# Kernel optimization log

Measured on AMD Instinct MI355X. Metric: run time of the kernel, lower is better.

## Reference

```python
import jax, jax.numpy as jnp
import numpy as np

N_NODES = 50000
N_EDGES = 800000
NFEAT, NHID, NCLASS = 256, 64, 40


def setup_inputs() -> dict:
    key = jax.random.key(0)
    ks = jax.random.split(key, 8)
    x = jax.random.normal(ks[0], (N_NODES, NFEAT), dtype=jnp.float32)
    W1 = jax.random.normal(ks[1], (NFEAT, NHID), dtype=jnp.float32) * (1.0 / np.sqrt(NFEAT))
    b1 = jax.random.normal(ks[2], (NHID,), dtype=jnp.float32) * 0.01
    W2 = jax.random.normal(ks[3], (NHID, NCLASS), dtype=jnp.float32) * (1.0 / np.sqrt(NHID))
    b2 = jax.random.normal(ks[4], (NCLASS,), dtype=jnp.float32) * 0.01
    edge_weight = jax.random.uniform(ks[5], (N_EDGES,), dtype=jnp.float32)
    edge_src = jax.random.randint(ks[6], (N_EDGES,), 0, N_NODES)
    edge_dst = jax.random.randint(ks[7], (N_EDGES,), 0, N_NODES)
    return {"x": x, "W1": W1, "b1": b1, "W2": W2, "b2": b2,
            "edge_weight": edge_weight, "edge_src": edge_src, "edge_dst": edge_dst}


def reference(x, W1, b1, W2, b2, edge_weight, edge_src, edge_dst):
    n = x.shape[0]

    def spmm(h):  # sparse adj @ h via gather + weighted segment-sum
        msgs = h[edge_src] * edge_weight[:, None]  # [E, d]
        return jax.ops.segment_sum(msgs, edge_dst, num_segments=n)

    # gc1: adj @ (x @ W1) + b1, then relu (dropout is identity in eval mode)
    h = jax.nn.relu(spmm(x @ W1) + b1)
    # gc2: adj @ (h @ W2) + b2
    logits = spmm(h @ W2) + b2
    return (logits, jax.nn.log_softmax(logits, axis=1))
```

## Files before the change

kernel.cpp:

```cpp
#include <hip/hip_runtime.h>
#include <math.h>

#define N_NODES 50000
#define N_EDGES 800000
#define NFEAT 256
#define NHID 64
#define NCLASS 40
#define NPB 16
#define NB  3125
#define CAP 512
#define NC 98
#define CAPC 16384
#define BIN_EPB 8192
#define NBIN 98
#define NGEMM 782
#define ACC2S 68

typedef __attribute__((ext_vector_type(8))) short bf16x8;
typedef __attribute__((ext_vector_type(4))) float f32x4;

__device__ __forceinline__ ushort f2bf(float f) {
    unsigned u = __float_as_uint(f);
    u += 0x7FFF + ((u >> 16) & 1);
    return (ushort)(u >> 16);
}
__device__ __forceinline__ float bf2f(ushort us) {
    return __uint_as_float(((unsigned)us) << 16);
}

__global__ __launch_bounds__(256) void k_prep(const float* __restrict__ W1,
                                              const float* __restrict__ W2,
                                              ushort* __restrict__ W1f,
                                              ushort* __restrict__ W2f) {
    int idx = blockIdx.x * 256 + threadIdx.x;
    if (idx < 2048) {
        int lane = idx & 63, ctks = idx >> 6;
        int ks = ctks & 7, ct = ctks >> 3;
        int col = ct * 16 + (lane & 15);
        int r0 = ks * 32 + (lane >> 4) * 8;
        bf16x8 frag;
        #pragma unroll
        for (int j = 0; j < 8; ++j) frag[j] = (short)f2bf(W1[(r0 + j) * NHID + col]);
        *(bf16x8*)&W1f[(size_t)idx * 8] = frag;
    } else if (idx < 2048 + 384) {
        int i2 = idx - 2048;
        int lane = i2 & 63, ctks = i2 >> 6;
        int ks = ctks & 1, ct = ctks >> 1;
        int col = ct * 16 + (lane & 15);
        int r0 = ks * 32 + (lane >> 4) * 8;
        bf16x8 frag;
        #pragma unroll
        for (int j = 0; j < 8; ++j)
            frag[j] = (short)((col < NCLASS) ? f2bf(W2[(r0 + j) * NCLASS + col]) : 0);
        *(bf16x8*)&W2f[(size_t)i2 * 8] = frag;
    }
}

__global__ __launch_bounds__(1024) void k_mega(const int* __restrict__ esrc,
                                               const int* __restrict__ edst,
                                               const float* __restrict__ ewt,
                                               int* __restrict__ bfillc,
                                               int2* __restrict__ coarse,
                                               const float* __restrict__ x,
                                               const ushort* __restrict__ W1f,
                                               ushort* __restrict__ xW1b) {
    __shared__ __align__(16) char smem[64 * 256 * 2];
    int tid = threadIdx.x;

    if (blockIdx.x < NBIN) {
        int* cnt  = (int*)smem;
        int* base = cnt + NC;
        for (int i = tid; i < NC; i += 1024) cnt[i] = 0;
        __syncthreads();
        int eb = blockIdx.x * BIN_EPB;
        #pragma unroll
        for (int k = 0; k < BIN_EPB; k += 1024) {
            int e = eb + k + tid;
            if (e < N_EDGES) atomicAdd(&cnt[edst[e] >> 9], 1);
        }
        __syncthreads();
        for (int i = tid; i < NC; i += 1024) {
            int c = cnt[i];
            base[i] = c ? atomicAdd(&bfillc[i], c) : 0;
            cnt[i] = 0;
        }
        __syncthreads();
        #pragma unroll
        for (int k = 0; k < BIN_EPB; k += 1024) {
            int e = eb + k + tid;
            if (e < N_EDGES) {
                int d = edst[e];
                int c = d >> 9;
                int pos = base[c] + atomicAdd(&cnt[c], 1);
                coarse[(size_t)c * CAPC + pos] =
                    make_int2(esrc[e] | ((d & 511) << 16), __float_as_int(ewt[e]));
            }
        }
        return;
    }

    ushort* sX = (ushort*)smem;
    int w = tid >> 6, lane = tid & 63;
    int ct = w & 3, rg = w >> 2;
    int row0 = (blockIdx.x - NBIN) * 64;

    bf16x8 Bf[8];
    #pragma unroll
    for (int ks = 0; ks < 8; ++ks)
        Bf[ks] = *(const bf16x8*)&W1f[(size_t)((ct * 8 + ks) * 64 + lane) * 8];

    {
        int row = tid & 63;
        int colbase = (tid >> 6) * 16;
        int crow = min(row0 + row, N_NODES - 1);
        const float* xp = x + (size_t)crow * NFEAT + colbase;
        #pragma unroll
        for (int c2 = 0; c2 < 2; ++c2) {
            float4 v0 = *(const float4*)(xp + c2 * 8);
            float4 v1 = *(const float4*)(xp + c2 * 8 + 4);
            bf16x8 fr;
            fr[0] = (short)f2bf(v0.x); fr[1] = (short)f2bf(v0.y);
            fr[2] = (short)f2bf(v0.z); fr[3] = (short)f2bf(v0.w);
            fr[4] = (short)f2bf(v1.x); fr[5] = (short)f2bf(v1.y);
            fr[6] = (short)f2bf(v1.z); fr[7] = (short)f2bf(v1.w);
            int chunk = colbase / 8 + c2;
            *(bf16x8*)&sX[row * 256 + ((chunk ^ (row & 7)) * 8)] = fr;
        }
    }
    __syncthreads();

    f32x4 acc = {0.f, 0.f, 0.f, 0.f};
    int arow = rg * 16 + (lane & 15);
    #pragma unroll
    for (int ks = 0; ks < 8; ++ks) {
        int chunk = ks * 4 + (lane >> 4);
        bf16x8 Af = *(const bf16x8*)&sX[arow * 256 + ((chunk ^ (arow & 7)) * 8)];
        acc = __builtin_amdgcn_mfma_f32_16x16x32_bf16(Af, Bf[ks], acc, 0, 0, 0);
    }
    int col = ct * 16 + (lane & 15);
    int rbase = row0 + rg * 16 + (lane >> 4) * 4;
    #pragma unroll
    for (int r = 0; r < 4; ++r) {
        int row = rbase + r;
        if (row < N_NODES)
            xW1b[(size_t)row * NHID + col] = f2bf(acc[r]);
    }
}

__global__ __launch_bounds__(512) void k_passB(const int* __restrict__ bfillc,
                                               const int2* __restrict__ coarse,
                                               int* __restrict__ bfill,
                                               int2* __restrict__ binned) {
    __shared__ int cnt[32];
    __shared__ int base[32];
    int tid = threadIdx.x;
    int c = blockIdx.x >> 1;
    int half = blockIdx.x & 1;
    int fillc = bfillc[c];
    int h0 = (fillc + 1) >> 1;
    int js = c * CAPC + half * h0;
    int je = c * CAPC + (half ? fillc : h0);

    if (tid < 32) cnt[tid] = 0;
    __syncthreads();
    for (int j = js + tid; j < je; j += 512) {
        int dstlow = (coarse[j].x >> 16) & 511;
        atomicAdd(&cnt[dstlow >> 4], 1);
    }
    __syncthreads();
    if (tid < 32) {
        int cc = cnt[tid];
        base[tid] = cc ? atomicAdd(&bfill[c * 32 + tid], cc) : 0;
        cnt[tid] = 0;
    }
    __syncthreads();
    for (int j = js + tid; j < je; j += 512) {
        int2 p = coarse[j];
        int dstlow = (p.x >> 16) & 511;
        int fb = dstlow >> 4;
        int pos = base[fb] + atomicAdd(&cnt[fb], 1);
        binned[(size_t)(c * 32 + fb) * CAP + pos] =
            make_int2((p.x & 0xFFFF) | ((dstlow & 15) << 16), p.y);
    }
}

__global__ __launch_bounds__(256) void k_spmm1b(const ushort* __restrict__ xW1b,
                                                const int* __restrict__ bfill,
                                                const int2* __restrict__ binned,
                                                const float* __restrict__ b1,
                                                ushort* __restrict__ h_b) {
    __shared__ float accs[4][NPB * NHID];
    int wv = threadIdx.x >> 6, lane = threadIdx.x & 63;
    int b = blockIdx.x;
    float* acc = accs[wv];
    #pragma unroll
    for (int n = 0; n < NPB; ++n) acc[n * NHID + lane] = 0.f;

    int s = b * CAP, e = s + bfill[b];
    int len = e - s;
    int q = (len + 3) >> 2;
    int j = s + wv * q;
    int je = min(j + q, e);
    for (; j + 8 <= je; j += 8) {
        int2 p[8];
        #pragma unroll
        for (int k = 0; k < 8; ++k) p[k] = binned[j + k];
        float g[8];
        #pragma unroll
        for (int k = 0; k < 8; ++k)
            g[k] = bf2f(xW1b[(p[k].x & 0xFFFF) * NHID + lane]);
        #pragma unroll
        for (int k = 0; k < 8; ++k)
            acc[(p[k].x >> 16) * NHID + lane] += __int_as_float(p[k].y) * g[k];
    }
    for (; j < je; ++j) {
        int2 p0 = binned[j];
        float g0 = bf2f(xW1b[(p0.x & 0xFFFF) * NHID + lane]);
        acc[(p0.x >> 16) * NHID + lane] += __int_as_float(p0.y) * g0;
    }
    __syncthreads();

    float bias = b1[lane];
    #pragma unroll
    for (int i = 0; i < 4; ++i) {
        int n = wv * 4 + i;
        float v = accs[0][n * NHID + lane] + accs[1][n * NHID + lane]
                + accs[2][n * NHID + lane] + accs[3][n * NHID + lane] + bias;
        h_b[(size_t)(b * NPB + n) * NHID + lane] = f2bf(v > 0.f ? v : 0.f);
    }
}

__global__ __launch_bounds__(256) void k_spmm2f(const ushort* __restrict__ h_b,
                                                const int* __restrict__ bfill,
                                                const int2* __restrict__ binned,
                                                const ushort* __restrict__ W2f,
                                                const float* __restrict__ b2,
                                                float* __restrict__ out) {
    __shared__ float accs[4][NPB * ACC2S];
    int wv = threadIdx.x >> 6, lane = threadIdx.x & 63;
    int b = blockIdx.x;
    float* acc = accs[wv];
    #pragma unroll
    for (int n = 0; n < NPB; ++n) acc[n * ACC2S + lane] = 0.f;

    int s = b * CAP, e = s + bfill[b];
    int len = e - s;
    int q = (len + 3) >> 2;
    int j = s + wv * q;
    int je = min(j + q, e);
    for (; j + 8 <= je; j += 8) {
        int2 p[8];
        #pragma unroll
        for (int k = 0; k < 8; ++k) p[k] = binned[j + k];
        float g[8];
        #pragma unroll
        for (int k = 0; k < 8; ++k)
            g[k] = bf2f(h_b[(p[k].x & 0xFFFF) * NHID + lane]);
        #pragma unroll
        for (int k = 0; k < 8; ++k)
            acc[(p[k].x >> 16) * ACC2S + lane] += __int_as_float(p[k].y) * g[k];
    }
    for (; j < je; ++j) {
        int2 p0 = binned[j];
        float g0 = bf2f(h_b[(p0.x & 0xFFFF) * NHID + lane]);
        acc[(p0.x >> 16) * ACC2S + lane] += __int_as_float(p0.y) * g0;
    }
    __syncthreads();

    for (int i = threadIdx.x; i < NPB * 64; i += 256) {
        int idx = (i >> 6) * ACC2S + (i & 63);
        accs[0][idx] = accs[0][idx] + accs[1][idx] + accs[2][idx] + accs[3][idx];
    }
    __syncthreads();
    if (wv != 0) return;

    bf16x8 Af[2];
    #pragma unroll
    for (int ks = 0; ks < 2; ++ks) {
        const float* ap = &accs[0][(lane & 15) * ACC2S + ks * 32 + (lane >> 4) * 8];
        #pragma unroll
        for (int jj = 0; jj < 8; ++jj) Af[ks][jj] = (short)f2bf(ap[jj]);
    }
    f32x4 cv[3] = {{0.f,0.f,0.f,0.f},{0.f,0.f,0.f,0.f},{0.f,0.f,0.f,0.f}};
    #pragma unroll
    for (int ct = 0; ct < 3; ++ct) {
        #pragma unroll
        for (int ks = 0; ks < 2; ++ks) {
            bf16x8 Bf = *(const bf16x8*)&W2f[(size_t)((ct * 2 + ks) * 64 + lane) * 8];
            cv[ct] = __builtin_amdgcn_mfma_f32_16x16x32_bf16(Af[ks], Bf, cv[ct], 0, 0, 0);
        }
    }
    int colg = lane & 15;
    int g = lane >> 4;
    float bc0 = b2[colg];
    float bc1 = b2[16 + colg];
    float bc2 = (colg < 8) ? b2[32 + colg] : 0.f;
    #pragma unroll
    for (int i = 0; i < 4; ++i) {
        int node = b * NPB + g * 4 + i;
        float v0 = cv[0][i] + bc0;
        float v1 = cv[1][i] + bc1;
        float v2 = (colg < 8) ? (cv[2][i] + bc2) : -INFINITY;
        float m = fmaxf(fmaxf(v0, v1), v2);
        #pragma unroll
        for (int off = 1; off < 16; off <<= 1) m = fmaxf(m, __shfl_xor(m, off));
        float ex = __expf(v0 - m) + __expf(v1 - m) + ((colg < 8) ? __expf(v2 - m) : 0.f);
        #pragma unroll
        for (int off = 1; off < 16; off <<= 1) ex += __shfl_xor(ex, off);
        float ls = __logf(ex) + m;
        float* o0 = out + (size_t)node * NCLASS;
        float* o1 = o0 + (size_t)N_NODES * NCLASS;
        o0[colg] = v0;            o1[colg] = v0 - ls;
        o0[16 + colg] = v1;       o1[16 + colg] = v1 - ls;
        if (colg < 8) { o0[32 + colg] = v2;  o1[32 + colg] = v2 - ls; }
    }
}


extern "C" void kernel_launch(void* const* d_in, const int* in_sizes, int n_in,
                              void* d_out, int out_size, void* d_ws, size_t ws_size,
                              hipStream_t stream) {
    const float* x    = (const float*)d_in[0];
    const float* W1   = (const float*)d_in[1];
    const float* b1   = (const float*)d_in[2];
    const float* W2   = (const float*)d_in[3];
    const float* b2   = (const float*)d_in[4];
    const float* ewt  = (const float*)d_in[5];
    const int*   esrc = (const int*)d_in[6];
    const int*   edst = (const int*)d_in[7];
    float* out = (float*)d_out;

    char* p = (char*)d_ws;
    ushort* xW1b = (ushort*)p;   p += (size_t)N_NODES * NHID * 2;
    ushort* h_b  = (ushort*)p;   p += (size_t)N_NODES * NHID * 2;
    int2*   binned = (int2*)p;   p += (size_t)NB * CAP * 8 + 64;
    int2*   coarse = (int2*)p;   p += (size_t)NC * CAPC * 8;
    ushort* W1f  = (ushort*)p;   p += 2048 * 8 * 2;
    ushort* W2f  = (ushort*)p;   p += 384 * 8 * 2;
    int* bfillc  = (int*)p;      p += NC * 4;
    int* bfill   = (int*)p;      p += NB * 4;

    hipMemsetAsync(bfillc, 0, (NC + NB) * sizeof(int), stream);

    k_prep<<<10, 256, 0, stream>>>(W1, W2, W1f, W2f);
    k_mega<<<NBIN + NGEMM, 1024, 0, stream>>>(esrc, edst, ewt, bfillc, coarse,
                                              x, W1f, xW1b);
    k_passB<<<NC * 2, 512, 0, stream>>>(bfillc, coarse, bfill, binned);
    k_spmm1b<<<NB, 256, 0, stream>>>(xW1b, bfill, binned, b1, h_b);
    k_spmm2f<<<NB, 256, 0, stream>>>(h_b, bfill, binned, W2f, b2, out);
}
```

Measured before the change: 189.4 us.

## Apply W2 before second SpMM to shrink gathered feature width

The h@W2 projection moves out of the second SpMM epilogue and into the first SpMM's epilogue, using MFMA. It writes a 48-wide bf16 hW2 (40 classes padded) instead of the 64-wide h. The second SpMM then gathers 48-column rows, which cuts gather bytes per edge, and it performs bias plus log_softmax with a wave-wide reduction. The cost is an extra MFMA stage in spmm1, one more block barrier, and padded lanes that still load (clamped to column 0) in spmm2.

```diff
diff --git a/kernel.cpp b/kernel.cpp
--- a/kernel.cpp
+++ b/kernel.cpp
@@ -14,7 +14,8 @@
 #define BIN_EPB 8192
 #define NBIN 98
 #define NGEMM 782
-#define ACC2S 68
+#define NW2 48
+#define ACC1S 68
 
 typedef __attribute__((ext_vector_type(8))) short bf16x8;
 typedef __attribute__((ext_vector_type(4))) float f32x4;
@@ -188,13 +189,14 @@
                                                 const int* __restrict__ bfill,
                                                 const int2* __restrict__ binned,
                                                 const float* __restrict__ b1,
-                                                ushort* __restrict__ h_b) {
-    __shared__ float accs[4][NPB * NHID];
+                                                const ushort* __restrict__ W2f,
+                                                ushort* __restrict__ hW2b) {
+    __shared__ float accs[4][NPB * ACC1S];
     int wv = threadIdx.x >> 6, lane = threadIdx.x & 63;
     int b = blockIdx.x;
     float* acc = accs[wv];
     #pragma unroll
-    for (int n = 0; n < NPB; ++n) acc[n * NHID + lane] = 0.f;
+    for (int n = 0; n < NPB; ++n) acc[n * ACC1S + lane] = 0.f;
 
     int s = b * CAP, e = s + bfill[b];
     int len = e - s;
@@ -211,12 +213,12 @@
             g[k] = bf2f(xW1b[(p[k].x & 0xFFFF) * NHID + lane]);
         #pragma unroll
         for (int k = 0; k < 8; ++k)
-            acc[(p[k].x >> 16) * NHID + lane] += __int_as_float(p[k].y) * g[k];
+            acc[(p[k].x >> 16) * ACC1S + lane] += __int_as_float(p[k].y) * g[k];
     }
     for (; j < je; ++j) {
         int2 p0 = binned[j];
         float g0 = bf2f(xW1b[(p0.x & 0xFFFF) * NHID + lane]);
-        acc[(p0.x >> 16) * NHID + lane] += __int_as_float(p0.y) * g0;
+        acc[(p0.x >> 16) * ACC1S + lane] += __int_as_float(p0.y) * g0;
     }
     __syncthreads();
 
@@ -224,24 +226,53 @@
     #pragma unroll
     for (int i = 0; i < 4; ++i) {
         int n = wv * 4 + i;
-        float v = accs[0][n * NHID + lane] + accs[1][n * NHID + lane]
-                + accs[2][n * NHID + lane] + accs[3][n * NHID + lane] + bias;
-        h_b[(size_t)(b * NPB + n) * NHID + lane] = f2bf(v > 0.f ? v : 0.f);
-    }
-}
-
-__global__ __launch_bounds__(256) void k_spmm2f(const ushort* __restrict__ h_b,
+        int idx = n * ACC1S + lane;
+        float v = accs[0][idx] + accs[1][idx] + accs[2][idx] + accs[3][idx] + bias;
+        accs[0][idx] = v > 0.f ? v : 0.f;
+    }
+    __syncthreads();
+    if (wv != 0) return;
+
+    bf16x8 Af[2];
+    #pragma unroll
+    for (int ks = 0; ks < 2; ++ks) {
+        const float* ap = &accs[0][(lane & 15) * ACC1S + ks * 32 + (lane >> 4) * 8];
+        #pragma unroll
+        for (int jj = 0; jj < 8; ++jj) Af[ks][jj] = (short)f2bf(ap[jj]);
+    }
+    f32x4 cv[3] = {{0.f,0.f,0.f,0.f},{0.f,0.f,0.f,0.f},{0.f,0.f,0.f,0.f}};
+    #pragma unroll
+    for (int ct = 0; ct < 3; ++ct) {
+        #pragma unroll
+        for (int ks = 0; ks < 2; ++ks) {
+            bf16x8 Bf = *(const bf16x8*)&W2f[(size_t)((ct * 2 + ks) * 64 + lane) * 8];
+            cv[ct] = __builtin_amdgcn_mfma_f32_16x16x32_bf16(Af[ks], Bf, cv[ct], 0, 0, 0);
+        }
+    }
+    int colg = lane & 15;
+    int g = lane >> 4;
+    #pragma unroll
+    for (int i = 0; i < 4; ++i) {
+        int node = b * NPB + g * 4 + i;
+        ushort* o = hW2b + (size_t)node * NW2;
+        o[colg]      = f2bf(cv[0][i]);
+        o[16 + colg] = f2bf(cv[1][i]);
+        o[32 + colg] = f2bf(cv[2][i]);
+    }
+}
+
+__global__ __launch_bounds__(256) void k_spmm2g(const ushort* __restrict__ hW2b,
                                                 const int* __restrict__ bfill,
                                                 const int2* __restrict__ binned,
-                                                const ushort* __restrict__ W2f,
                                                 const float* __restrict__ b2,
                                                 float* __restrict__ out) {
-    __shared__ float accs[4][NPB * ACC2S];
+    __shared__ float accs[4][NPB * 64];
     int wv = threadIdx.x >> 6, lane = threadIdx.x & 63;
     int b = blockIdx.x;
     float* acc = accs[wv];
-    #pragma unroll
-    for (int n = 0; n < NPB; ++n) acc[n * ACC2S + lane] = 0.f;
+    int lf = lane < NW2 ? lane : 0;
+    #pragma unroll
+    for (int n = 0; n < NPB; ++n) acc[n * 64 + lane] = 0.f;
 
     int s = b * CAP, e = s + bfill[b];
     int len = e - s;
@@ -255,64 +286,38 @@
         float g[8];
         #pragma unroll
         for (int k = 0; k < 8; ++k)
-            g[k] = bf2f(h_b[(p[k].x & 0xFFFF) * NHID + lane]);
+            g[k] = bf2f(hW2b[(p[k].x & 0xFFFF) * NW2 + lf]);
         #pragma unroll
         for (int k = 0; k < 8; ++k)
-            acc[(p[k].x >> 16) * ACC2S + lane] += __int_as_float(p[k].y) * g[k];
+            acc[(p[k].x >> 16) * 64 + lane] += __int_as_float(p[k].y) * g[k];
     }
     for (; j < je; ++j) {
         int2 p0 = binned[j];
-        float g0 = bf2f(h_b[(p0.x & 0xFFFF) * NHID + lane]);
-        acc[(p0.x >> 16) * ACC2S + lane] += __int_as_float(p0.y) * g0;
-    }
-    __syncthreads();
-
-    for (int i = threadIdx.x; i < NPB * 64; i += 256) {
-        int idx = (i >> 6) * ACC2S + (i & 63);
-        accs[0][idx] = accs[0][idx] + accs[1][idx] + accs[2][idx] + accs[3][idx];
-    }
-    __syncthreads();
-    if (wv != 0) return;
-
-    bf16x8 Af[2];
-    #pragma unroll
-    for (int ks = 0; ks < 2; ++ks) {
-        const float* ap = &accs[0][(lane & 15) * ACC2S + ks * 32 + (lane >> 4) * 8];
-        #pragma unroll
-        for (int jj = 0; jj < 8; ++jj) Af[ks][jj] = (short)f2bf(ap[jj]);
-    }
-    f32x4 cv[3] = {{0.f,0.f,0.f,0.f},{0.f,0.f,0.f,0.f},{0.f,0.f,0.f,0.f}};
-    #pragma unroll
-    for (int ct = 0; ct < 3; ++ct) {
-        #pragma unroll
-        for (int ks = 0; ks < 2; ++ks) {
-            bf16x8 Bf = *(const bf16x8*)&W2f[(size_t)((ct * 2 + ks) * 64 + lane) * 8];
-            cv[ct] = __builtin_amdgcn_mfma_f32_16x16x32_bf16(Af[ks], Bf, cv[ct], 0, 0, 0);
-        }
-    }
-    int colg = lane & 15;
-    int g = lane >> 4;
-    float bc0 = b2[colg];
-    float bc1 = b2[16 + colg];
-    float bc2 = (colg < 8) ? b2[32 + colg] : 0.f;
+        float g0 = bf2f(hW2b[(p0.x & 0xFFFF) * NW2 + lf]);
+        acc[(p0.x >> 16) * 64 + lane] += __int_as_float(p0.y) * g0;
+    }
+    __syncthreads();
+
+    float bias = (lane < NCLASS) ? b2[lane] : 0.f;
     #pragma unroll
     for (int i = 0; i < 4; ++i) {
-        int node = b * NPB + g * 4 + i;
-        float v0 = cv[0][i] + bc0;
-        float v1 = cv[1][i] + bc1;
-        float v2 = (colg < 8) ? (cv[2][i] + bc2) : -INFINITY;
-        float m = fmaxf(fmaxf(v0, v1), v2);
-        #pragma unroll
-        for (int off = 1; off < 16; off <<= 1) m = fmaxf(m, __shfl_xor(m, off));
-        float ex = __expf(v0 - m) + __expf(v1 - m) + ((colg < 8) ? __expf(v2 - m) : 0.f);
-        #pragma unroll
-        for (int off = 1; off < 16; off <<= 1) ex += __shfl_xor(ex, off);
-        float ls = __logf(ex) + m;
-        float* o0 = out + (size_t)node * NCLASS;
-        float* o1 = o0 + (size_t)N_NODES * NCLASS;
-        o0[colg] = v0;            o1[colg] = v0 - ls;
-        o0[16 + colg] = v1;       o1[16 + colg] = v1 - ls;
-        if (colg < 8) { o0[32 + colg] = v2;  o1[32 + colg] = v2 - ls; }
+        int n = wv * 4 + i;
+        float vs = accs[0][n * 64 + lane] + accs[1][n * 64 + lane]
+                 + accs[2][n * 64 + lane] + accs[3][n * 64 + lane];
+        float v = (lane < NCLASS) ? (vs + bias) : -INFINITY;
+        float m = v;
+        #pragma unroll
+        for (int off = 32; off; off >>= 1) m = fmaxf(m, __shfl_xor(m, off));
+        float ex = (lane < NCLASS) ? __expf(v - m) : 0.f;
+        float ssum = ex;
+        #pragma unroll
+        for (int off = 32; off; off >>= 1) ssum += __shfl_xor(ssum, off);
+        float ls = __logf(ssum);
+        if (lane < NCLASS) {
+            int node = b * NPB + n;
+            out[(size_t)node * NCLASS + lane] = v;
+            out[(size_t)N_NODES * NCLASS + (size_t)node * NCLASS + lane] = v - m - ls;
+        }
     }
 }
 
@@ -332,7 +337,7 @@
 
     char* p = (char*)d_ws;
     ushort* xW1b = (ushort*)p;   p += (size_t)N_NODES * NHID * 2;
-    ushort* h_b  = (ushort*)p;   p += (size_t)N_NODES * NHID * 2;
+    ushort* hW2b = (ushort*)p;   p += (size_t)N_NODES * NW2 * 2;
     int2*   binned = (int2*)p;   p += (size_t)NB * CAP * 8 + 64;
     int2*   coarse = (int2*)p;   p += (size_t)NC * CAPC * 8;
     ushort* W1f  = (ushort*)p;   p += 2048 * 8 * 2;
@@ -346,6 +351,6 @@
     k_mega<<<NBIN + NGEMM, 1024, 0, stream>>>(esrc, edst, ewt, bfillc, coarse,
                                               x, W1f, xW1b);
     k_passB<<<NC * 2, 512, 0, stream>>>(bfillc, coarse, bfill, binned);
-    k_spmm1b<<<NB, 256, 0, stream>>>(xW1b, bfill, binned, b1, h_b);
-    k_spmm2f<<<NB, 256, 0, stream>>>(h_b, bfill, binned, W2f, b2, out);
-}
+    k_spmm1b<<<NB, 256, 0, stream>>>(xW1b, bfill, binned, b1, W2f, hW2b);
+    k_spmm2g<<<NB, 256, 0, stream>>>(hW2b, bfill, binned, b2, out);
+}
```

Measured after the change: 197.2 us. +4.1%, slower.
